# Performance work log

Hardware: AMD Instinct MI355X
Metric: run time of the kernel (lower is better)

## Reference

```python
import jax, jax.numpy as jnp
import numpy as np

B, N, D = 8, 4096, 1024
S, K = 4, 16            # n_slices, per-slice codebook size (2^(16/4))
d = D // S              # slice_dim = 256
BETA = 0.25


def setup_inputs() -> dict:
    key = jax.random.key(0)
    k1, k2 = jax.random.split(key)
    h = jax.random.normal(k1, (B, N, D), dtype=jnp.float32)
    # nn.init.uniform_(codebook.weight, -1/K, 1/K)
    codebooks = jax.random.uniform(k2, (S, K, d), dtype=jnp.float32,
                                   minval=-1.0 / K, maxval=1.0 / K)
    return {"h": h, "codebooks": codebooks}


def reference(h, codebooks):
    Bb, Nn, Dd = h.shape
    Ss, Kk, dd = codebooks.shape
    sg = jax.lax.stop_gradient

    # sliced DVQ: view h as [B,N,S,d]
    ze = h.reshape(Bb, Nn, Ss, dd)

    # pairwise squared distances per slice: [B,N,S,K]
    dist = ((ze ** 2).sum(-1, keepdims=True)
            + (codebooks ** 2).sum(-1)[None, None, :, :]
            - 2.0 * jnp.einsum('bnsd,skd->bnsk', ze, codebooks))
    ids = jnp.argmin(dist, axis=-1)                         # [B,N,S] int

    # gather nearest codes: [B,N,S,d]
    zq = codebooks[jnp.arange(Ss)[None, None, :], ids]

    # per-slice VQ losses (mse over that slice), summed over slices
    loss_cb = jnp.mean((zq - sg(ze)) ** 2, axis=(0, 1, 3))  # [S]
    loss_cm = jnp.mean((ze - sg(zq)) ** 2, axis=(0, 1, 3))  # [S]
    vq_total = (loss_cb + BETA * loss_cm).sum()

    # straight-through estimator, concat slices back to [B,N,D]
    z = (ze + sg(zq - ze)).reshape(Bb, Nn, Dd)

    # pack ids: offsets are [1, K, K^2, K^3] since all slice sizes equal
    offsets = (Kk ** jnp.arange(Ss)).astype(jnp.int32)
    ids_packed = (ids.astype(jnp.int32) * offsets).sum(-1)  # [B,N]

    return (z, ids_packed, vq_total)
```

## Files before the change

### kernel.cpp

```cpp
#include <hip/hip_runtime.h>


#define D_FULL 1024
#define SEG 4
#define DSEG 256
#define KC 16

__global__ __launch_bounds__(256) void dvq_prep(const float* __restrict__ cb,
                                                double* __restrict__ c2d,
                                                float* __restrict__ ids_out,
                                                float* __restrict__ loss_out) {
    __shared__ double ws[4];
    const int b = blockIdx.x;
    const int t = threadIdx.x;
    const int lane = t & 63;
    const int w = t >> 6;

    ids_out[b * 512 + t] = 0.0f;
    ids_out[b * 512 + 256 + t] = 0.0f;
    if (b == 0 && t == 0) *loss_out = 0.0f;

    double v = (double)cb[b * 256 + t];
    double sq = v * v;
#pragma unroll
    for (int off = 32; off > 0; off >>= 1)
        sq += __shfl_down(sq, off, 64);
    if (lane == 0) ws[w] = sq;
    __syncthreads();
    if (t == 0) c2d[b] = ws[0] + ws[1] + ws[2] + ws[3];
}

__global__ __launch_bounds__(256) void dvq_main(const float* __restrict__ h,
                                                const float* __restrict__ cb,
                                                const double* __restrict__ c2d,
                                                float* __restrict__ z_out,
                                                float* __restrict__ ids_out,
                                                float* __restrict__ loss_out) {
    __shared__ __align__(16) float4 hl[64 * 64];
    __shared__ __align__(16) float cbl[KC * DSEG];

    const int i = threadIdx.x;
    const int lane = i & 63;
    const int w = i >> 6;
    const int ch = __builtin_amdgcn_readfirstlane(w);

    const int s = blockIdx.x & 3;
    const long tok_base = (long)(blockIdx.x >> 2) * 64;

    {
        const float4* src = reinterpret_cast<const float4*>(cb + s * (KC * DSEG));
        float4* dst = reinterpret_cast<float4*>(cbl);
#pragma unroll
        for (int jj = 0; jj < 4; ++jj)
            dst[jj * 256 + i] = src[jj * 256 + i];
    }

    {
#pragma unroll
        for (int half = 0; half < 2; ++half) {
            float4 tmp[8];
#pragma unroll
            for (int rr = 0; rr < 8; ++rr) {
                const int r = ch * 16 + half * 8 + rr;
                tmp[rr] = *(const float4*)(h + (tok_base + r) * D_FULL +
                                           (long)s * DSEG + lane * 4);
            }
#pragma unroll
            for (int rr = 0; rr < 8; ++rr) {
                const int r = ch * 16 + half * 8 + rr;
                hl[r * 64 + (lane ^ r)] = tmp[rr];
            }
        }
    }
    __syncthreads();

    const float* cbs = cbl + ch * 64;
    const int tk = lane;

    double dot[KC];
#pragma unroll
    for (int k = 0; k < KC; ++k) dot[k] = 0.0;
    double ze2 = 0.0;

#pragma unroll 4
    for (int j = 0; j < 16; ++j) {
        const int jj = ch * 16 + j;
        float4 z4 = hl[tk * 64 + (jj ^ tk)];
        double z0 = (double)z4.x, z1 = (double)z4.y;
        double z2 = (double)z4.z, z3 = (double)z4.w;
        ze2 = fma(z0, z0, ze2);
        ze2 = fma(z1, z1, ze2);
        ze2 = fma(z2, z2, ze2);
        ze2 = fma(z3, z3, ze2);
#pragma unroll
        for (int k = 0; k < KC; ++k) {
            float4 c4 = *(const float4*)(cbs + k * DSEG + j * 4);
            double a = dot[k];
            a = fma(z0, (double)c4.x, a);
            a = fma(z1, (double)c4.y, a);
            a = fma(z2, (double)c4.z, a);
            a = fma(z3, (double)c4.w, a);
            dot[k] = a;
        }
    }

    __syncthreads();
    double* part = (double*)hl;
    int* ids_l = (int*)((char*)hl + 26112);
    if (w != 0) {
        double* p = part + ((w - 1) * 64 + lane) * (KC + 1);
#pragma unroll
        for (int k = 0; k < KC; ++k) p[k] = dot[k];
        p[KC] = ze2;
    }
    __syncthreads();

    if (w == 0) {
#pragma unroll
        for (int c = 0; c < 3; ++c) {
            const double* p = part + (c * 64 + lane) * (KC + 1);
#pragma unroll
            for (int k = 0; k < KC; ++k) dot[k] += p[k];
            ze2 += p[KC];
        }

        const double* c2s = c2d + s * KC;
        double best = c2s[0] - 2.0 * dot[0];
        int bk = 0;
#pragma unroll
        for (int k = 1; k < KC; ++k) {
            double sc = c2s[k] - 2.0 * dot[k];
            if (sc < best) { best = sc; bk = k; }
        }
        ids_l[lane] = bk;

        atomicAdd(&ids_out[tok_base + lane], (float)(bk << (4 * s)));

        double mind = ze2 + best;
#pragma unroll
        for (int off = 32; off > 0; off >>= 1)
            mind += __shfl_down(mind, off, 64);
        if (lane == 0)
            atomicAdd(loss_out, (float)(mind * (1.25 / 8388608.0)));
    }
    __syncthreads();

    const float4* cbl4 = (const float4*)cbl;
#pragma unroll 4
    for (int r0 = 0; r0 < 16; ++r0) {
        int r = ch * 16 + r0;
        int k = ids_l[r];
        float4 v = cbl4[k * 64 + lane];
        ((float4*)(z_out + (tok_base + r) * D_FULL + (long)s * DSEG))[lane] = v;
    }
}

extern "C" void kernel_launch(void* const* d_in, const int* in_sizes, int n_in,
                              void* d_out, int out_size, void* d_ws, size_t ws_size,
                              hipStream_t stream) {
    const float* h  = (const float*)d_in[0];
    const float* cb = (const float*)d_in[1];

    const int n_h = in_sizes[0];
    const int tokens = n_h / D_FULL;

    float* z_out    = (float*)d_out;
    float* ids_out  = z_out + (size_t)n_h;
    float* loss_out = ids_out + tokens;

    double* c2d = (double*)d_ws;

    dvq_prep<<<64, 256, 0, stream>>>(cb, c2d, ids_out, loss_out);
    dvq_main<<<(tokens / 64) * SEG, 256, 0, stream>>>(h, cb, c2d, z_out,
                                                      ids_out, loss_out);
}
```

Measured before the change: 270.1 us.

## Load tiles directly into LDS via global_load_lds and double threads per block

Replaces the register-staged global-to-LDS copies of the hidden tile and codebook slice with direct global_load_lds DMA instructions, keeping the XOR swizzle by permuting the source address. Blocks grow from 256 to 512 threads (8 waves), so each wave handles half as many feature chunks, and the partial-sum reduction now merges 7 waves instead of 3. This is meant to cut register pressure and load latency and to raise parallelism per tile, at the cost of a larger cross-wave reduction done by wave 0 and heavier LDS use for the partials.

```diff
diff --git a/kernel.cpp b/kernel.cpp
--- a/kernel.cpp
+++ b/kernel.cpp
@@ -5,6 +5,14 @@
 #define SEG 4
 #define DSEG 256
 #define KC 16
+
+#define GLOBAL_AS __attribute__((address_space(1)))
+#define LDS_AS __attribute__((address_space(3)))
+
+static __device__ __forceinline__ void load_lds16(const void* g, void* l) {
+    __builtin_amdgcn_global_load_lds((GLOBAL_AS const unsigned int*)g,
+                                     (LDS_AS unsigned int*)l, 16, 0, 0);
+}
 
 __global__ __launch_bounds__(256) void dvq_prep(const float* __restrict__ cb,
                                                 double* __restrict__ c2d,
@@ -30,12 +38,12 @@
     if (t == 0) c2d[b] = ws[0] + ws[1] + ws[2] + ws[3];
 }
 
-__global__ __launch_bounds__(256) void dvq_main(const float* __restrict__ h,
-                                                const float* __restrict__ cb,
-                                                const double* __restrict__ c2d,
-                                                float* __restrict__ z_out,
-                                                float* __restrict__ ids_out,
-                                                float* __restrict__ loss_out) {
+__global__ __launch_bounds__(512, 4) void dvq_main(const float* __restrict__ h,
+                                                   const float* __restrict__ cb,
+                                                   const double* __restrict__ c2d,
+                                                   float* __restrict__ z_out,
+                                                   float* __restrict__ ids_out,
+                                                   float* __restrict__ loss_out) {
     __shared__ __align__(16) float4 hl[64 * 64];
     __shared__ __align__(16) float cbl[KC * DSEG];
 
@@ -47,34 +55,25 @@
     const int s = blockIdx.x & 3;
     const long tok_base = (long)(blockIdx.x >> 2) * 64;
 
-    {
-        const float4* src = reinterpret_cast<const float4*>(cb + s * (KC * DSEG));
-        float4* dst = reinterpret_cast<float4*>(cbl);
+    char* hl_b = (char*)hl;
+    char* cbl_b = (char*)cbl;
+
 #pragma unroll
-        for (int jj = 0; jj < 4; ++jj)
-            dst[jj * 256 + i] = src[jj * 256 + i];
+    for (int rr = 0; rr < 8; ++rr) {
+        const int r = ch * 8 + rr;
+        load_lds16(h + (tok_base + r) * D_FULL + (long)s * DSEG +
+                       ((lane ^ r) << 2),
+                   hl_b + r * 1024);
+    }
+#pragma unroll
+    for (int half = 0; half < 2; ++half) {
+        load_lds16(cb + s * (KC * DSEG) + ch * 512 + half * 256 + lane * 4,
+                   cbl_b + ch * 2048 + half * 1024);
     }
 
-    {
-#pragma unroll
-        for (int half = 0; half < 2; ++half) {
-            float4 tmp[8];
-#pragma unroll
-            for (int rr = 0; rr < 8; ++rr) {
-                const int r = ch * 16 + half * 8 + rr;
-                tmp[rr] = *(const float4*)(h + (tok_base + r) * D_FULL +
-                                           (long)s * DSEG + lane * 4);
-            }
-#pragma unroll
-            for (int rr = 0; rr < 8; ++rr) {
-                const int r = ch * 16 + half * 8 + rr;
-                hl[r * 64 + (lane ^ r)] = tmp[rr];
-            }
-        }
-    }
     __syncthreads();
 
-    const float* cbs = cbl + ch * 64;
+    const float* cbs = cbl + ch * 32;
     const int tk = lane;
 
     double dot[KC];
@@ -82,9 +81,9 @@
     for (int k = 0; k < KC; ++k) dot[k] = 0.0;
     double ze2 = 0.0;
 
-#pragma unroll 4
-    for (int j = 0; j < 16; ++j) {
-        const int jj = ch * 16 + j;
+#pragma unroll
+    for (int j = 0; j < 8; ++j) {
+        const int jj = ch * 8 + j;
         float4 z4 = hl[tk * 64 + (jj ^ tk)];
         double z0 = (double)z4.x, z1 = (double)z4.y;
         double z2 = (double)z4.z, z3 = (double)z4.w;
@@ -106,7 +105,7 @@
 
     __syncthreads();
     double* part = (double*)hl;
-    int* ids_l = (int*)((char*)hl + 26112);
+    int* ids_l = (int*)((char*)hl + 60928);
     if (w != 0) {
         double* p = part + ((w - 1) * 64 + lane) * (KC + 1);
 #pragma unroll
@@ -117,7 +116,7 @@
 
     if (w == 0) {
 #pragma unroll
-        for (int c = 0; c < 3; ++c) {
+        for (int c = 0; c < 7; ++c) {
             const double* p = part + (c * 64 + lane) * (KC + 1);
 #pragma unroll
             for (int k = 0; k < KC; ++k) dot[k] += p[k];
@@ -146,9 +145,9 @@
     __syncthreads();
 
     const float4* cbl4 = (const float4*)cbl;
-#pragma unroll 4
-    for (int r0 = 0; r0 < 16; ++r0) {
-        int r = ch * 16 + r0;
+#pragma unroll
+    for (int r0 = 0; r0 < 8; ++r0) {
+        int r = ch * 8 + r0;
         int k = ids_l[r];
         float4 v = cbl4[k * 64 + lane];
         ((float4*)(z_out + (tok_base + r) * D_FULL + (long)s * DSEG))[lane] = v;
@@ -171,6 +170,6 @@
     double* c2d = (double*)d_ws;
 
     dvq_prep<<<64, 256, 0, stream>>>(cb, c2d, ids_out, loss_out);
-    dvq_main<<<(tokens / 64) * SEG, 256, 0, stream>>>(h, cb, c2d, z_out,
+    dvq_main<<<(tokens / 64) * SEG, 512, 0, stream>>>(h, cb, c2d, z_out,
                                                       ids_out, loss_out);
 }
```

Measured after the change: 243.0 us. 1.11x faster.
